# Performance work log

Hardware: AMD Instinct MI355X
Metric: run time of the kernel (lower is better)

The kernel has to match this reference:

```python
import jax, jax.numpy as jnp
import numpy as np

D_MODEL = 512
N_HEADS = 8
D_K = D_MODEL // N_HEADS
B, L = 4, 2048


def setup_inputs() -> dict:
    key = jax.random.key(0)
    ks = jax.random.split(key, 9)
    s = 1.0 / np.sqrt(D_MODEL)  # nn.Linear default init scale (uniform bound)
    def lin(kw, kb):
        W = jax.random.uniform(kw, (D_MODEL, D_MODEL), jnp.float32, -s, s)
        b = jax.random.uniform(kb, (D_MODEL,), jnp.float32, -s, s)
        return W, b
    Wq, bq = lin(ks[0], ks[1])
    Wk, bk = lin(ks[2], ks[3])
    Wv, bv = lin(ks[4], ks[5])
    return {
        "queries": jax.random.normal(ks[6], (B, L, D_MODEL), jnp.float32),
        "keys": jax.random.normal(ks[7], (B, L, D_MODEL), jnp.float32),
        "values": jax.random.normal(ks[8], (B, L, D_MODEL), jnp.float32),
        "Wq": Wq, "bq": bq, "Wk": Wk, "bk": bk, "Wv": Wv, "bv": bv,
    }


def reference(queries, keys, values, Wq, bq, Wk, bk, Wv, bv):
    # Torch Linear: y = x @ W.T + b; here W stored as [in, out] so y = x @ W + b
    Bsz, Lq, _ = queries.shape
    Lk = keys.shape[1]
    # project and split heads -> [B, H, L, d_k]
    Q = (queries @ Wq + bq).reshape(Bsz, Lq, N_HEADS, D_K).transpose(0, 2, 1, 3)
    K = (keys @ Wk + bk).reshape(Bsz, Lk, N_HEADS, D_K).transpose(0, 2, 1, 3)
    V = (values @ Wv + bv).reshape(Bsz, Lk, N_HEADS, D_K).transpose(0, 2, 1, 3)
    scores = jnp.einsum("bhqd,bhkd->bhqk", Q, K) / np.sqrt(D_K).astype(np.float32)
    attn_weights = jax.nn.softmax(scores, axis=-1)  # dropout is identity in eval
    out = jnp.einsum("bhqk,bhkd->bhqd", attn_weights, V)
    out = out.transpose(0, 2, 1, 3).reshape(Bsz, Lq, D_MODEL)
    return out, attn_weights
```

## Files before the change

### kernel.cpp

```cpp
#include <hip/hip_runtime.h>
#include <hip/hip_bf16.h>


using u16 = unsigned short;
using u32 = unsigned int;

typedef __attribute__((ext_vector_type(4))) float  f32x4;
typedef __attribute__((ext_vector_type(8))) short  s16x8;
typedef __attribute__((ext_vector_type(4))) short  s16x4;
typedef __attribute__((ext_vector_type(2))) unsigned int u32x2;
typedef __attribute__((ext_vector_type(4))) unsigned int u32x4;

#define MFMA16(a,b,c) __builtin_amdgcn_mfma_f32_16x16x32_bf16(a,b,c,0,0,0)

#if __has_builtin(__builtin_amdgcn_mfma_f32_16x16x16bf16_1k)
#define MFMA1616(a,b,c) __builtin_amdgcn_mfma_f32_16x16x16bf16_1k(a,b,c,0,0,0)
#else
__device__ __forceinline__ f32x4 MFMA1616(s16x4 a, s16x4 b, f32x4 c){
  asm("v_mfma_f32_16x16x16_bf16 %0, %1, %2, %0" : "+v"(c) : "v"(a), "v"(b));
  return c;
}
#endif

__device__ __forceinline__ u16 f2bf(float f){
  u32 x; __builtin_memcpy(&x, &f, 4);
  x += 0x7FFFu + ((x >> 16) & 1u);
  return (u16)(x >> 16);
}
__device__ __forceinline__ u32 pk2(float a, float b){
  return (u32)f2bf(a) | ((u32)f2bf(b) << 16);
}
#if __has_builtin(__builtin_amdgcn_exp2f)
__device__ __forceinline__ float ex2(float x){ return __builtin_amdgcn_exp2f(x); }
#else
__device__ __forceinline__ float ex2(float x){ return exp2f(x); }
#endif

__device__ __forceinline__ void async16(const u16* src, char* wavebase, int lane){
#if __has_builtin(__builtin_amdgcn_global_load_lds)
  __builtin_amdgcn_global_load_lds(
      (const __attribute__((address_space(1))) unsigned int*)src,
      (__attribute__((address_space(3))) unsigned int*)wavebase, 16, 0, 0);
#else
  *(u32x4*)(wavebase + lane*16) = *(const u32x4*)src;
#endif
}

#define SCALE2 0.18033688f

__global__ void wt_kernel(const float* __restrict__ W0, const float* __restrict__ W1,
                          const float* __restrict__ W2,
                          u16* __restrict__ T0, u16* __restrict__ T1, u16* __restrict__ T2){
  const float* W = blockIdx.z==0 ? W0 : (blockIdx.z==1 ? W1 : W2);
  u16*         T = blockIdx.z==0 ? T0 : (blockIdx.z==1 ? T1 : T2);
  __shared__ u16 t[32][33];
  int x = threadIdx.x, y0 = threadIdx.y;
  int bx = blockIdx.x*32, by = blockIdx.y*32;
  #pragma unroll
  for (int i=0;i<4;i++){ int y=y0+i*8; t[y][x] = f2bf(W[(by+y)*512 + bx + x]); }
  __syncthreads();
  #pragma unroll
  for (int i=0;i<4;i++){ int y=y0+i*8; T[(bx+y)*512 + by + x] = t[x][y]; }
}

__global__ __launch_bounds__(256,2) void proj_kernel(
    const float* __restrict__ q_in, const float* __restrict__ k_in, const float* __restrict__ v_in,
    const u16* __restrict__ Wt,
    const float* __restrict__ bq, const float* __restrict__ bk, const float* __restrict__ bv,
    u16* __restrict__ Qo, u16* __restrict__ Ko, u16* __restrict__ Vto)
{
  const int mode = blockIdx.z;
  const int lt = blockIdx.x;
  const int nt = blockIdx.y;
  const float* Xf   = mode==0 ? q_in : (mode==1 ? k_in : v_in);
  const u16*   Wm   = Wt + (size_t)mode*512*512;
  const float* bias = mode==0 ? bq : (mode==1 ? bk : bv);

  __shared__ __align__(16) u16 As[128*32];
  __shared__ __align__(16) u16 Bs[128*32];

  u16* Wdst = (mode<2) ? As : Bs;
  u16* Xdst = (mode<2) ? Bs : As;
  const int wrow0 = nt*128, xrow0 = lt*128;

  const int t = threadIdx.x;
  const int w = t>>6, lane = t&63, l16 = lane&15, quad = lane>>4;
  const int am = (w&1)*64, bn = (w>>1)*64;

  f32x4 acc[4][4];
  #pragma unroll
  for (int i=0;i<4;i++)
    #pragma unroll
    for (int j=0;j<4;j++) acc[i][j] = (f32x4){0.f,0.f,0.f,0.f};

  for (int kk=0; kk<512; kk+=32){
    __syncthreads();
    #pragma unroll
    for (int j=0;j<2;j++){
      int id = j*256 + t;
      int row = id>>2, c4 = id&3;
      int sw = c4 ^ (row&3) ^ ((row>>2)&3);
      u32x4 vw = *(const u32x4*)(Wm + (size_t)(wrow0+row)*512 + kk + c4*8);
      *(u32x4*)((char*)Wdst + row*64 + sw*16) = vw;
      const float* xp = Xf + (size_t)(xrow0+row)*512 + kk + c4*8;
      f32x4 x0 = *(const f32x4*)xp;
      f32x4 x1 = *(const f32x4*)(xp+4);
      u32x4 vx = { pk2(x0[0],x0[1]), pk2(x0[2],x0[3]),
                   pk2(x1[0],x1[1]), pk2(x1[2],x1[3]) };
      *(u32x4*)((char*)Xdst + row*64 + sw*16) = vx;
    }
    __syncthreads();
    s16x8 fa[4], fb[4];
    #pragma unroll
    for (int i=0;i<4;i++){
      int ra = am + i*16 + l16;
      fa[i] = *(const s16x8*)((const char*)As + ra*64 + ((quad ^ (ra&3) ^ ((ra>>2)&3))*16));
      int rb = bn + i*16 + l16;
      fb[i] = *(const s16x8*)((const char*)Bs + rb*64 + ((quad ^ (rb&3) ^ ((rb>>2)&3))*16));
    }
    #pragma unroll
    for (int i=0;i<4;i++)
      #pragma unroll
      for (int j=0;j<4;j++)
        acc[i][j] = MFMA16(fa[i], fb[j], acc[i][j]);
  }

  if (mode < 2){
    u16* Out = mode==0 ? Qo : Ko;
    #pragma unroll
    for (int i=0;i<4;i++){
      int n0 = nt*128 + am + i*16 + quad*4;
      float b4[4];
      #pragma unroll
      for (int r=0;r<4;r++) b4[r] = bias[n0+r];
      int h = n0>>6, d0 = n0&63;
      #pragma unroll
      for (int j=0;j<4;j++){
        int lg = lt*128 + bn + j*16 + l16;
        int b = lg>>11, ll = lg&2047;
        u32x2 pk = { pk2(acc[i][j][0]+b4[0], acc[i][j][1]+b4[1]),
                     pk2(acc[i][j][2]+b4[2], acc[i][j][3]+b4[3]) };
        *(u32x2*)(Out + ((size_t)(((b<<3)+h)*2048 + ll)<<6) + d0) = pk;
      }
    }
  } else {
    #pragma unroll
    for (int j=0;j<4;j++){
      int nv = nt*128 + bn + j*16 + l16;
      float bvv = bias[nv];
      int h = nv>>6, d = nv&63;
      #pragma unroll
      for (int i=0;i<4;i++){
        int lg = lt*128 + am + i*16 + quad*4;
        int b = lg>>11, ll = lg&2047;
        u32x2 pk = { pk2(acc[i][j][0]+bvv, acc[i][j][1]+bvv),
                     pk2(acc[i][j][2]+bvv, acc[i][j][3]+bvv) };
        *(u32x2*)(Vto + ((size_t)(((b<<3)+h)*64 + d)<<11) + ll) = pk;
      }
    }
  }
}

__global__ __launch_bounds__(512,4) void attn_kernel(
    const u16* __restrict__ Q, const u16* __restrict__ K, const u16* __restrict__ Vt,
    float* __restrict__ out, float* __restrict__ attn)
{
  const int qt = blockIdx.x;
  const int bh = blockIdx.z*8 + blockIdx.y;
  const int q0 = qt*128;
  const u16* Qg = Q  + (size_t)bh*2048*64;
  const u16* Kg = K  + (size_t)bh*2048*64;
  const u16* Vg = Vt + (size_t)bh*64*2048;
  float* attng = attn + ((size_t)bh*2048 + q0)*2048;

  __shared__ __align__(128) char smem[65536];
  float* Ls = (float*)(smem + 49152);
  float* Os = (float*)smem;

  const int t = threadIdx.x;
  const int w = t>>6, lane = t&63, l16 = lane&15, quad = lane>>4;
  const int coff = (w&1)*64, roff = (w>>1)*32;

  if (t < 128) Ls[t] = 0.f;
  __syncthreads();

  s16x8 qf[2][2];
  #pragma unroll
  for (int kc=0;kc<2;kc++)
    #pragma unroll
    for (int ri=0;ri<2;ri++)
      qf[kc][ri] = *(const s16x8*)(Qg + (size_t)(q0 + roff + ri*16 + l16)*64 + (kc*4+quad)*8);

  #pragma unroll
  for (int j=0;j<2;j++){
    int id = j*512 + t; int row = id>>3, ch = id&7;
    async16(Kg + (size_t)row*64 + ((ch ^ (row&7))*8), smem + (j*512 + w*64)*16, lane);
  }
  #pragma unroll
  for (int j=0;j<2;j++){
    int id = j*512 + t; int row = id>>4, ch = id&15;
    async16(Vg + (size_t)row*2048 + ((ch ^ (row&15))*8), smem + 32768 + (j*512 + w*64)*16, lane);
  }

  float lsum[2] = {0.f, 0.f};
  for (int kt=0; kt<16; kt++){
    f32x4 s[4][2];
    #pragma unroll
    for (int ci=0;ci<4;ci++)
      #pragma unroll
      for (int ri=0;ri<2;ri++) s[ci][ri] = (f32x4){0.f,0.f,0.f,0.f};
    #pragma unroll
    for (int kc=0;kc<2;kc++){
      #pragma unroll
      for (int ci=0;ci<4;ci++){
        int rc = kt*128 + coff + ci*16 + l16;
        s16x8 fa = *(const s16x8*)(Kg + (size_t)rc*64 + (kc*4+quad)*8);
        #pragma unroll
        for (int ri=0;ri<2;ri++) s[ci][ri] = MFMA16(fa, qf[kc][ri], s[ci][ri]);
      }
    }
    #pragma unroll
    for (int ri=0;ri<2;ri++){
      float ps = 0.f;
      #pragma unroll
      for (int ci=0;ci<4;ci++)
        #pragma unroll
        for (int r=0;r<4;r++) ps += ex2(s[ci][ri][r]*SCALE2);
      lsum[ri] += ps;
    }
  }
  #pragma unroll
  for (int ri=0;ri<2;ri++){
    float v = lsum[ri];
    v += __shfl_xor(v, 16, 64);
    v += __shfl_xor(v, 32, 64);
    if (quad == 0) atomicAdd(&Ls[roff + ri*16 + l16], v);
  }
  __syncthreads();
  float rinv[2];
  #pragma unroll
  for (int ri=0;ri<2;ri++) rinv[ri] = 1.0f / Ls[roff + ri*16 + l16];
  __syncthreads();

  f32x4 o[2][4];
  #pragma unroll
  for (int ri=0;ri<2;ri++)
    #pragma unroll
    for (int ni=0;ni<4;ni++) o[ri][ni] = (f32x4){0.f,0.f,0.f,0.f};

  int cur = 0;
  for (int kt=0; kt<16; kt++){
    char* Kc = smem + cur*16384;
    char* Vc = smem + 32768 + cur*16384;
    char* Kn = smem + (cur^1)*16384;
    char* Vn = smem + 32768 + (cur^1)*16384;
    if (kt < 15){
      #pragma unroll
      for (int j=0;j<2;j++){
        int id = j*512 + t; int row = id>>3, ch = id&7;
        async16(Kg + (size_t)((kt+1)*128+row)*64 + ((ch ^ (row&7))*8),
                Kn + (j*512 + w*64)*16, lane);
      }
      #pragma unroll
      for (int j=0;j<2;j++){
        int id = j*512 + t; int row = id>>4, ch = id&15;
        async16(Vg + (size_t)row*2048 + (kt+1)*128 + ((ch ^ (row&15))*8),
                Vn + (j*512 + w*64)*16, lane);
      }
    }
    f32x4 s[4][2];
    #pragma unroll
    for (int ci=0;ci<4;ci++)
      #pragma unroll
      for (int ri=0;ri<2;ri++) s[ci][ri] = (f32x4){0.f,0.f,0.f,0.f};
    #pragma unroll
    for (int kc=0;kc<2;kc++){
      #pragma unroll
      for (int ci=0;ci<4;ci++){
        int rc = coff + ci*16 + l16;
        s16x8 fa = *(const s16x8*)(Kc + rc*128 + (((kc*4+quad) ^ (rc&7))*16));
        #pragma unroll
        for (int ri=0;ri<2;ri++) s[ci][ri] = MFMA16(fa, qf[kc][ri], s[ci][ri]);
      }
    }
    s16x4 pa[4][2];
    #pragma unroll
    for (int ci=0;ci<4;ci++){
      #pragma unroll
      for (int ri=0;ri<2;ri++){
        f32x4 e;
        #pragma unroll
        for (int r=0;r<4;r++) e[r] = ex2(s[ci][ri][r]*SCALE2)*rinv[ri];
        int rr = roff + ri*16 + l16;
        int c0 = coff + ci*16 + quad*4;
        *(f32x4*)(attng + (size_t)rr*2048 + kt*128 + c0) = e;
        s16x4 p;
        #pragma unroll
        for (int r=0;r<4;r++) p[r] = (short)f2bf(e[r]);
        pa[ci][ri] = p;
      }
    }
    #pragma unroll
    for (int cc=0;cc<4;cc++){
      #pragma unroll
      for (int ni=0;ni<4;ni++){
        int dd = ni*16 + l16;
        int ch = ((coff>>3) + cc*2 + (quad>>1)) ^ (dd&15);
        s16x4 vb = *(const s16x4*)(Vc + dd*256 + ch*16 + (quad&1)*8);
        #pragma unroll
        for (int ri=0;ri<2;ri++) o[ri][ni] = MFMA1616(pa[cc][ri], vb, o[ri][ni]);
      }
    }
    __syncthreads();
    cur ^= 1;
  }

  if (w & 1){
    #pragma unroll
    for (int ri=0;ri<2;ri++)
      #pragma unroll
      for (int ni=0;ni<4;ni++)
        #pragma unroll
        for (int r=0;r<4;r++)
          Os[(roff + ri*16 + quad*4 + r)*68 + ni*16 + l16] = o[ri][ni][r];
  }
  __syncthreads();
  if (!(w & 1)){
    float* og = out + ((size_t)(bh>>3)*2048 + q0)*512 + (bh&7)*64;
    #pragma unroll
    for (int ri=0;ri<2;ri++)
      #pragma unroll
      for (int ni=0;ni<4;ni++)
        #pragma unroll
        for (int r=0;r<4;r++){
          int rr = roff + ri*16 + quad*4 + r;
          int dd = ni*16 + l16;
          og[(size_t)rr*512 + dd] = o[ri][ni][r] + Os[rr*68 + dd];
        }
  }
}

extern "C" void kernel_launch(void* const* d_in, const int* in_sizes, int n_in,
                              void* d_out, int out_size, void* d_ws, size_t ws_size,
                              hipStream_t stream) {
  (void)in_sizes; (void)n_in; (void)out_size; (void)ws_size;
  const float* q_in = (const float*)d_in[0];
  const float* k_in = (const float*)d_in[1];
  const float* v_in = (const float*)d_in[2];
  const float* Wq   = (const float*)d_in[3];
  const float* bq   = (const float*)d_in[4];
  const float* Wk   = (const float*)d_in[5];
  const float* bk   = (const float*)d_in[6];
  const float* Wv   = (const float*)d_in[7];
  const float* bv   = (const float*)d_in[8];

  u16* ws  = (u16*)d_ws;
  u16* Wt  = ws;
  u16* Qw  = ws + 786432;
  u16* Kw  = Qw + 4194304;
  u16* Vtw = Kw + 4194304;

  float* outp  = (float*)d_out;
  float* attnp = outp + 4194304;

  wt_kernel  <<<dim3(16,16,3), dim3(32,8), 0, stream>>>(Wq, Wk, Wv, Wt, Wt+262144, Wt+524288);
  proj_kernel<<<dim3(64,4,3),  256,       0, stream>>>(q_in, k_in, v_in, Wt, bq, bk, bv, Qw, Kw, Vtw);
  attn_kernel<<<dim3(16,8,4),  512,       0, stream>>>(Qw, Kw, Vtw, outp, attnp);
}
```

Before: 700.3 us.

## Pre-convert inputs to bf16, async-load projection tiles, fold softmax normalization into exp

A new prep kernel merges the weight transpose with a bulk fp32-to-bf16 conversion of the activations into workspace. The projection GEMM then streams both operands into LDS through async global-to-LDS loads with a swizzled source address, and its occupancy hint rises to 4. In attention, K fragments are loaded before the MFMA block, which runs at raised wave priority. Softmax normalization becomes an fma with -log2(sum) inside exp2, and the P·V step is interleaved per column chunk to lower register pressure. The cost is an extra full write and read of the bf16 activation copy through memory.

```diff
diff --git a/kernel.cpp b/kernel.cpp
--- a/kernel.cpp
+++ b/kernel.cpp
@@ -48,40 +48,53 @@
 
 #define SCALE2 0.18033688f
 
-__global__ void wt_kernel(const float* __restrict__ W0, const float* __restrict__ W1,
-                          const float* __restrict__ W2,
-                          u16* __restrict__ T0, u16* __restrict__ T1, u16* __restrict__ T2){
-  const float* W = blockIdx.z==0 ? W0 : (blockIdx.z==1 ? W1 : W2);
-  u16*         T = blockIdx.z==0 ? T0 : (blockIdx.z==1 ? T1 : T2);
-  __shared__ u16 t[32][33];
-  int x = threadIdx.x, y0 = threadIdx.y;
-  int bx = blockIdx.x*32, by = blockIdx.y*32;
-  #pragma unroll
-  for (int i=0;i<4;i++){ int y=y0+i*8; t[y][x] = f2bf(W[(by+y)*512 + bx + x]); }
-  __syncthreads();
-  #pragma unroll
-  for (int i=0;i<4;i++){ int y=y0+i*8; T[(bx+y)*512 + by + x] = t[x][y]; }
-}
-
-__global__ __launch_bounds__(256,2) void proj_kernel(
+__global__ __launch_bounds__(256) void prep_kernel(
+    const float* __restrict__ Wq, const float* __restrict__ Wk, const float* __restrict__ Wv,
     const float* __restrict__ q_in, const float* __restrict__ k_in, const float* __restrict__ v_in,
-    const u16* __restrict__ Wt,
+    u16* __restrict__ Wt, u16* __restrict__ Xb)
+{
+  const int b = blockIdx.x, t = threadIdx.x;
+  if (b < 768){
+    int zi = b >> 8, rem = b & 255;
+    const float* W = zi==0 ? Wq : (zi==1 ? Wk : Wv);
+    u16*         T = Wt + zi*262144;
+    __shared__ u16 tls[32][33];
+    int x = t & 31, y0 = t >> 5;
+    int bx = (rem & 15)*32, by = (rem >> 4)*32;
+    #pragma unroll
+    for (int i=0;i<4;i++){ int y=y0+i*8; tls[y][x] = f2bf(W[(by+y)*512 + bx + x]); }
+    __syncthreads();
+    #pragma unroll
+    for (int i=0;i<4;i++){ int y=y0+i*8; T[(bx+y)*512 + by + x] = tls[x][y]; }
+  } else {
+    int g = (b - 768)*256 + t;
+    int mode = g >> 19, off = g & 524287;
+    const float* src = mode==0 ? q_in : (mode==1 ? k_in : v_in);
+    const float* sp = src + (size_t)off*8;
+    f32x4 a = *(const f32x4*)sp;
+    f32x4 c = *(const f32x4*)(sp+4);
+    u32x4 o = { pk2(a[0],a[1]), pk2(a[2],a[3]), pk2(c[0],c[1]), pk2(c[2],c[3]) };
+    *(u32x4*)(Xb + (size_t)mode*4194304 + (size_t)off*8) = o;
+  }
+}
+
+__global__ __launch_bounds__(256,4) void proj_kernel(
+    const u16* __restrict__ Xb, const u16* __restrict__ Wt,
     const float* __restrict__ bq, const float* __restrict__ bk, const float* __restrict__ bv,
     u16* __restrict__ Qo, u16* __restrict__ Ko, u16* __restrict__ Vto)
 {
   const int mode = blockIdx.z;
   const int lt = blockIdx.x;
   const int nt = blockIdx.y;
-  const float* Xf   = mode==0 ? q_in : (mode==1 ? k_in : v_in);
-  const u16*   Wm   = Wt + (size_t)mode*512*512;
+  const u16* Xm = Xb + (size_t)mode*4194304;
+  const u16* Wm = Wt + (size_t)mode*262144;
   const float* bias = mode==0 ? bq : (mode==1 ? bk : bv);
 
   __shared__ __align__(16) u16 As[128*32];
   __shared__ __align__(16) u16 Bs[128*32];
 
-  u16* Wdst = (mode<2) ? As : Bs;
-  u16* Xdst = (mode<2) ? Bs : As;
-  const int wrow0 = nt*128, xrow0 = lt*128;
+  const u16* Ab = (mode<2) ? Wm : Xm;  const int Ar0 = (mode<2) ? nt*128 : lt*128;
+  const u16* Bb = (mode<2) ? Xm : Wm;  const int Br0 = (mode<2) ? lt*128 : nt*128;
 
   const int t = threadIdx.x;
   const int w = t>>6, lane = t&63, l16 = lane&15, quad = lane>>4;
@@ -96,18 +109,18 @@
   for (int kk=0; kk<512; kk+=32){
     __syncthreads();
     #pragma unroll
-    for (int j=0;j<2;j++){
-      int id = j*256 + t;
-      int row = id>>2, c4 = id&3;
-      int sw = c4 ^ (row&3) ^ ((row>>2)&3);
-      u32x4 vw = *(const u32x4*)(Wm + (size_t)(wrow0+row)*512 + kk + c4*8);
-      *(u32x4*)((char*)Wdst + row*64 + sw*16) = vw;
-      const float* xp = Xf + (size_t)(xrow0+row)*512 + kk + c4*8;
-      f32x4 x0 = *(const f32x4*)xp;
-      f32x4 x1 = *(const f32x4*)(xp+4);
-      u32x4 vx = { pk2(x0[0],x0[1]), pk2(x0[2],x0[3]),
-                   pk2(x1[0],x1[1]), pk2(x1[2],x1[3]) };
-      *(u32x4*)((char*)Xdst + row*64 + sw*16) = vx;
+    for (int h=0;h<2;h++){
+      int cidx = (w*2+h)*64 + lane;
+      int row = cidx>>2, s4 = cidx&3;
+      int c4 = s4 ^ (row&3) ^ ((row>>2)&3);
+      async16(Ab + (size_t)(Ar0+row)*512 + kk + c4*8, (char*)As + (w*2+h)*1024, lane);
+    }
+    #pragma unroll
+    for (int h=0;h<2;h++){
+      int cidx = (w*2+h)*64 + lane;
+      int row = cidx>>2, s4 = cidx&3;
+      int c4 = s4 ^ (row&3) ^ ((row>>2)&3);
+      async16(Bb + (size_t)(Br0+row)*512 + kk + c4*8, (char*)Bs + (w*2+h)*1024, lane);
     }
     __syncthreads();
     s16x8 fa[4], fb[4];
@@ -211,13 +224,19 @@
       for (int ri=0;ri<2;ri++) s[ci][ri] = (f32x4){0.f,0.f,0.f,0.f};
     #pragma unroll
     for (int kc=0;kc<2;kc++){
+      s16x8 fa[4];
       #pragma unroll
       for (int ci=0;ci<4;ci++){
         int rc = kt*128 + coff + ci*16 + l16;
-        s16x8 fa = *(const s16x8*)(Kg + (size_t)rc*64 + (kc*4+quad)*8);
-        #pragma unroll
-        for (int ri=0;ri<2;ri++) s[ci][ri] = MFMA16(fa, qf[kc][ri], s[ci][ri]);
-      }
+        fa[ci] = *(const s16x8*)(Kg + (size_t)rc*64 + (kc*4+quad)*8);
+      }
+      __builtin_amdgcn_s_setprio(1);
+      #pragma unroll
+      for (int ci=0;ci<4;ci++)
+        #pragma unroll
+        for (int ri=0;ri<2;ri++)
+          s[ci][ri] = MFMA16(fa[ci], qf[kc][ri], s[ci][ri]);
+      __builtin_amdgcn_s_setprio(0);
     }
     #pragma unroll
     for (int ri=0;ri<2;ri++){
@@ -237,9 +256,9 @@
     if (quad == 0) atomicAdd(&Ls[roff + ri*16 + l16], v);
   }
   __syncthreads();
-  float rinv[2];
-  #pragma unroll
-  for (int ri=0;ri<2;ri++) rinv[ri] = 1.0f / Ls[roff + ri*16 + l16];
+  float nm2[2];
+  #pragma unroll
+  for (int ri=0;ri<2;ri++) nm2[ri] = -__log2f(Ls[roff + ri*16 + l16]);
   __syncthreads();
 
   f32x4 o[2][4];
@@ -275,40 +294,43 @@
       for (int ri=0;ri<2;ri++) s[ci][ri] = (f32x4){0.f,0.f,0.f,0.f};
     #pragma unroll
     for (int kc=0;kc<2;kc++){
+      s16x8 fa[4];
       #pragma unroll
       for (int ci=0;ci<4;ci++){
         int rc = coff + ci*16 + l16;
-        s16x8 fa = *(const s16x8*)(Kc + rc*128 + (((kc*4+quad) ^ (rc&7))*16));
-        #pragma unroll
-        for (int ri=0;ri<2;ri++) s[ci][ri] = MFMA16(fa, qf[kc][ri], s[ci][ri]);
-      }
-    }
-    s16x4 pa[4][2];
-    #pragma unroll
-    for (int ci=0;ci<4;ci++){
+        fa[ci] = *(const s16x8*)(Kc + rc*128 + (((kc*4+quad) ^ (rc&7))*16));
+      }
+      __builtin_amdgcn_s_setprio(1);
+      #pragma unroll
+      for (int ci=0;ci<4;ci++)
+        #pragma unroll
+        for (int ri=0;ri<2;ri++)
+          s[ci][ri] = MFMA16(fa[ci], qf[kc][ri], s[ci][ri]);
+      __builtin_amdgcn_s_setprio(0);
+    }
+    #pragma unroll
+    for (int cc=0;cc<4;cc++){
+      s16x4 pa[2];
       #pragma unroll
       for (int ri=0;ri<2;ri++){
         f32x4 e;
         #pragma unroll
-        for (int r=0;r<4;r++) e[r] = ex2(s[ci][ri][r]*SCALE2)*rinv[ri];
+        for (int r=0;r<4;r++) e[r] = ex2(__builtin_fmaf(s[cc][ri][r], SCALE2, nm2[ri]));
         int rr = roff + ri*16 + l16;
-        int c0 = coff + ci*16 + quad*4;
+        int c0 = coff + cc*16 + quad*4;
         *(f32x4*)(attng + (size_t)rr*2048 + kt*128 + c0) = e;
         s16x4 p;
         #pragma unroll
         for (int r=0;r<4;r++) p[r] = (short)f2bf(e[r]);
-        pa[ci][ri] = p;
-      }
-    }
-    #pragma unroll
-    for (int cc=0;cc<4;cc++){
+        pa[ri] = p;
+      }
       #pragma unroll
       for (int ni=0;ni<4;ni++){
         int dd = ni*16 + l16;
         int ch = ((coff>>3) + cc*2 + (quad>>1)) ^ (dd&15);
         s16x4 vb = *(const s16x4*)(Vc + dd*256 + ch*16 + (quad&1)*8);
         #pragma unroll
-        for (int ri=0;ri<2;ri++) o[ri][ni] = MFMA1616(pa[cc][ri], vb, o[ri][ni]);
+        for (int ri=0;ri<2;ri++) o[ri][ni] = MFMA1616(pa[ri], vb, o[ri][ni]);
       }
     }
     __syncthreads();
@@ -359,11 +381,12 @@
   u16* Qw  = ws + 786432;
   u16* Kw  = Qw + 4194304;
   u16* Vtw = Kw + 4194304;
+  u16* Xb  = Vtw + 4194304;
 
   float* outp  = (float*)d_out;
   float* attnp = outp + 4194304;
 
-  wt_kernel  <<<dim3(16,16,3), dim3(32,8), 0, stream>>>(Wq, Wk, Wv, Wt, Wt+262144, Wt+524288);
-  proj_kernel<<<dim3(64,4,3),  256,       0, stream>>>(q_in, k_in, v_in, Wt, bq, bk, bv, Qw, Kw, Vtw);
-  attn_kernel<<<dim3(16,8,4),  512,       0, stream>>>(Qw, Kw, Vtw, outp, attnp);
-}
+  prep_kernel<<<6912, 256, 0, stream>>>(Wq, Wk, Wv, q_in, k_in, v_in, Wt, Xb);
+  proj_kernel<<<dim3(64,4,3), 256, 0, stream>>>(Xb, Wt, bq, bk, bv, Qw, Kw, Vtw);
+  attn_kernel<<<dim3(16,8,4), 512, 0, stream>>>(Qw, Kw, Vtw, outp, attnp);
+}
```

New measurement: 723.0 us. 3.2% more time.
